# Kernel optimization log

Measured on AMD Instinct MI355X. Metric: run time of the kernel, lower is better.

## Reference

```python
import jax, jax.numpy as jnp
import numpy as np

HEADS = 2
BN_EPS = 1e-5


def _upsample2x_bilinear_ac(x):
    # torch nn.Upsample(scale_factor=2, mode='bilinear', align_corners=True)
    B, C, H, W = x.shape

    def grid(n):
        c = jnp.arange(2 * n) * ((n - 1) / (2 * n - 1))  # align_corners mapping
        i0 = jnp.clip(jnp.floor(c).astype(jnp.int32), 0, n - 2)
        w = (c - i0).astype(x.dtype)
        return i0, w

    i0, wh = grid(H)
    j0, ww = grid(W)
    x = x[:, :, i0, :] * (1 - wh)[None, None, :, None] + x[:, :, i0 + 1, :] * wh[None, None, :, None]
    x = x[:, :, :, j0] * (1 - ww) + x[:, :, :, j0 + 1] * ww
    return x


def _self_attn(x, wq, wkv, wo, wob):
    # x: (b, t, d); lucidrains axial_attention SelfAttention
    b, t, d = x.shape
    e = d // HEADS
    q = x @ wq
    k, v = jnp.split(x @ wkv, 2, axis=-1)
    mh = lambda z: z.reshape(b, t, HEADS, e).transpose(0, 2, 1, 3)  # (b,h,t,e)
    q, k, v = mh(q), mh(k), mh(v)
    dots = jnp.einsum('bhie,bhje->bhij', q, k) * (e ** -0.5)
    attn = jax.nn.softmax(dots, axis=-1)
    o = jnp.einsum('bhij,bhje->bhie', attn, v)
    o = o.transpose(0, 2, 1, 3).reshape(b, t, d)
    return o @ wo + wob


def setup_inputs() -> dict:
    key = jax.random.key(0)
    ks = jax.random.split(key, 16)
    C, E = 256, 128
    cat = 2 * C + E
    s = 0.02
    inp = {
        'x': jax.random.normal(ks[0], (4, C, 64, 64), jnp.float32),
        'res': jax.random.normal(ks[1], (4, E, 128, 128), jnp.float32),
        'wq_h': jax.random.normal(ks[2], (C, C), jnp.float32) * s,
        'wkv_h': jax.random.normal(ks[3], (C, 2 * C), jnp.float32) * s,
        'wo_h': jax.random.normal(ks[4], (C, C), jnp.float32) * s,
        'wob_h': jnp.zeros((C,), jnp.float32),
        'wq_w': jax.random.normal(ks[5], (C, C), jnp.float32) * s,
        'wkv_w': jax.random.normal(ks[6], (C, 2 * C), jnp.float32) * s,
        'wo_w': jax.random.normal(ks[7], (C, C), jnp.float32) * s,
        'wob_w': jnp.zeros((C,), jnp.float32),
        'conv_w': jax.random.normal(ks[8], (cat, E), jnp.float32) * s,
        'gamma': jnp.ones((E,), jnp.float32),
        'beta': jnp.zeros((E,), jnp.float32),
    }
    return inp


def reference(x, res, wq_h, wkv_h, wo_h, wob_h, wq_w, wkv_w, wo_w, wob_w, conv_w, gamma, beta):
    xu = _upsample2x_bilinear_ac(x)  # (B,C,2H,2W)
    B, C, H, W = xu.shape
    # axial attention along H (rows): batch over B*W
    ah = xu.transpose(0, 3, 2, 1).reshape(B * W, H, C)
    ah = _self_attn(ah, wq_h, wkv_h, wo_h, wob_h).reshape(B, W, H, C).transpose(0, 3, 2, 1)
    # axial attention along W (cols): batch over B*H
    aw = xu.transpose(0, 2, 3, 1).reshape(B * H, W, C)
    aw = _self_attn(aw, wq_w, wkv_w, wo_w, wob_w).reshape(B, H, W, C).transpose(0, 3, 1, 2)
    x_attn = jax.nn.relu(ah + aw)  # sum_axial_out=True, then ReLU
    cat = jnp.concatenate([x_attn, xu, res], axis=1)  # (B, 2C+E, H, W)
    y = jnp.einsum('bchw,ce->behw', cat, conv_w)  # conv1x1, no bias
    y = jax.nn.relu(y)
    # BatchNorm2d, training-mode batch stats (biased variance)
    mu = y.mean(axis=(0, 2, 3), keepdims=True)
    var = y.var(axis=(0, 2, 3), keepdims=True)
    y = (y - mu) / jnp.sqrt(var + BN_EPS)
    return y * gamma[None, :, None, None] + beta[None, :, None, None]
```

## Files before the change

kernel.cpp:

```cpp
#include <hip/hip_runtime.h>
#include <hip/hip_bf16.h>
#include <cstdio>


typedef short bf16x8 __attribute__((ext_vector_type(8)));
typedef short bf16x4 __attribute__((ext_vector_type(4)));
typedef float f32x4 __attribute__((ext_vector_type(4)));

#define MFMA16(a, b, c) __builtin_amdgcn_mfma_f32_16x16x32_bf16((a), (b), (c), 0, 0, 0)

__device__ __forceinline__ short f2bf(float v) {
  __hip_bfloat16 h = __float2bfloat16(v);
  union { __hip_bfloat16 h; short s; } u; u.h = h; return u.s;
}
__device__ __forceinline__ float bf2f(short s) {
  return __uint_as_float(((unsigned int)(unsigned short)s) << 16);
}
__device__ __forceinline__ int swz(int row, int col) {
  return col ^ ((row & 7) << 3);
}

struct WtAll {
  const float* src[7];
  short* dst[7];
  int K[7], N[7], tile0[7];
};

__global__ __launch_bounds__(256) void k_wt_all(WtAll P) {
  const int bid = blockIdx.x;
  int i = 0;
#pragma unroll
  for (int j = 1; j < 7; j++) if (bid >= P.tile0[j]) i = j;
  const float* src = P.src[i];
  short* dst = P.dst[i];
  const int K = P.K[i], N = P.N[i];
  const int local = bid - P.tile0[i];
  const int ktiles = K >> 5;
  const int nt = local / ktiles, kt = local - nt * ktiles;
  const int k0 = kt * 32, n0 = nt * 32;
  __shared__ float tile[32][33];
  const int tx = threadIdx.x & 31, ty = threadIdx.x >> 5;
#pragma unroll
  for (int r = 0; r < 4; r++)
    tile[ty + r * 8][tx] = src[(size_t)(k0 + ty + r * 8) * N + n0 + tx];
  __syncthreads();
#pragma unroll
  for (int r = 0; r < 4; r++)
    dst[(size_t)(n0 + ty + r * 8) * K + k0 + tx] = f2bf(tile[tx][ty + r * 8]);
}

__global__ __launch_bounds__(256) void k_upsample(const float* __restrict__ x,
                                                  short* __restrict__ xu) {
  __shared__ float ldsV[64][65];
  const int bh = blockIdx.x, z = blockIdx.y;
  const int b = bh >> 7, h = bh & 127;
  const float chf = h * (63.0f / 127.0f);
  int i0 = (int)chf; if (i0 > 62) i0 = 62;
  const float wh = chf - (float)i0;
  const int t = threadIdx.x;
  const int cbase = z * 64;
  const float* xb = x + ((size_t)(b * 256 + cbase) * 64 + i0) * 64;
#pragma unroll
  for (int p = 0; p < 16; p++) {
    const int li = p * 256 + t;
    const int c = li >> 6, w = li & 63;
    const float* px = xb + (size_t)c * 4096 + w;
    const float v0 = px[0], v1 = px[64];
    ldsV[c][w] = v0 * (1.f - wh) + v1 * wh;
  }
  __syncthreads();
  const int cg = t & 7, wi = t >> 3;
  short* xout = xu + (size_t)(bh * 128) * 256 + cbase + cg * 8;
#pragma unroll
  for (int p = 0; p < 4; p++) {
    const int w = p * 32 + wi;
    const float cwf = w * (63.0f / 127.0f);
    int j0 = (int)cwf; if (j0 > 62) j0 = 62;
    const float ww = cwf - (float)j0;
    bf16x8 o;
#pragma unroll
    for (int u = 0; u < 8; u++) {
      const float v0 = ldsV[cg * 8 + u][j0], v1 = ldsV[cg * 8 + u][j0 + 1];
      o[u] = f2bf(v0 * (1.f - ww) + v1 * ww);
    }
    *(bf16x8*)(xout + (size_t)w * 256) = o;
  }
}

__global__ __launch_bounds__(512, 2) void k_fused(const short* __restrict__ xu,
                                                  const short* __restrict__ wqkvT,
                                                  const short* __restrict__ woT,
                                                  const float* __restrict__ wob,
                                                  short* __restrict__ accb,
                                                  int dir) {
  __shared__ __align__(16) short Xs[128][256];
  __shared__ __align__(16) short Qb[128][128];
  __shared__ __align__(16) short Kb[128][128];
  __shared__ __align__(16) short Vtb[128][128];

  const int s = blockIdx.x;
  const int b = s >> 7, pos = s & 127;
  const int tok0 = b * 16384 + (dir ? pos * 128 : pos);
  const int tstep = dir ? 1 : 128;
  const int tid = threadIdx.x;
  const int lane = tid & 63, wid = tid >> 6;
  const int lr = lane & 15, kb = lane >> 4;
  const int ct = wid * 16;
  const float scale = 0.08838834764831845f;

#pragma unroll
  for (int p = 0; p < 8; p++) {
    const int u = p * 512 + tid;
    const int row = u >> 5, ck = (u & 31) * 8;
    bf16x8 v = *(const bf16x8*)(xu + (size_t)(tok0 + row * tstep) * 256 + ck);
    *(bf16x8*)&Xs[row][swz(row, ck)] = v;
  }

  f32x4 accp[2][8];
#pragma unroll
  for (int i = 0; i < 2; i++)
#pragma unroll
    for (int j = 0; j < 8; j++) accp[i][j] = (f32x4){0.f, 0.f, 0.f, 0.f};

  for (int h = 0; h < 2; h++) {
    const short* wqb = wqkvT + (size_t)(h * 128 + ct + lr) * 256 + kb * 8;
    const short* wkb = wqkvT + (size_t)(256 + h * 128 + ct + lr) * 256 + kb * 8;
    const short* wvb = wqkvT + (size_t)(512 + h * 128 + ct + lr) * 256 + kb * 8;
    bf16x8 wq[8], wk[8], wv[8];
#pragma unroll
    for (int ks = 0; ks < 8; ks++) {
      wq[ks] = *(const bf16x8*)(wqb + ks * 32);
      wk[ks] = *(const bf16x8*)(wkb + ks * 32);
      wv[ks] = *(const bf16x8*)(wvb + ks * 32);
    }

    __syncthreads();

#pragma unroll
    for (int nt = 0; nt < 8; nt++) {
      const int xrow = nt * 16 + lr;
      f32x4 dq = (f32x4){0.f, 0.f, 0.f, 0.f};
      f32x4 dk = (f32x4){0.f, 0.f, 0.f, 0.f};
      f32x4 dv = (f32x4){0.f, 0.f, 0.f, 0.f};
#pragma unroll
      for (int ks = 0; ks < 8; ks++) {
        bf16x8 xf = *(const bf16x8*)&Xs[xrow][swz(xrow, kb * 8 + ks * 32)];
        dq = MFMA16(wq[ks], xf, dq);
        dk = MFMA16(wk[ks], xf, dk);
        dv = MFMA16(xf, wv[ks], dv);
      }
      const int trow = nt * 16 + lr, cc = ct + kb * 4;
      bf16x4 pq = {f2bf(dq[0]), f2bf(dq[1]), f2bf(dq[2]), f2bf(dq[3])};
      bf16x4 pk = {f2bf(dk[0]), f2bf(dk[1]), f2bf(dk[2]), f2bf(dk[3])};
      *(bf16x4*)&Qb[trow][swz(trow, cc)] = pq;
      *(bf16x4*)&Kb[trow][swz(trow, cc)] = pk;
      const int vrow = ct + lr;
      bf16x4 pv = {f2bf(dv[0]), f2bf(dv[1]), f2bf(dv[2]), f2bf(dv[3])};
      *(bf16x4*)&Vtb[vrow][swz(vrow, nt * 16 + kb * 4)] = pv;
    }

    __syncthreads();

    f32x4 s8[8];
#pragma unroll
    for (int i = 0; i < 8; i++) s8[i] = (f32x4){0.f, 0.f, 0.f, 0.f};
    const int qrow = ct + lr;
#pragma unroll
    for (int ks = 0; ks < 4; ks++) {
      bf16x8 aq = *(const bf16x8*)&Qb[qrow][swz(qrow, kb * 8 + ks * 32)];
#pragma unroll
      for (int nj = 0; nj < 8; nj++) {
        const int krow = nj * 16 + lr;
        bf16x8 bk = *(const bf16x8*)&Kb[krow][swz(krow, kb * 8 + ks * 32)];
        s8[nj] = MFMA16(bk, aq, s8[nj]);
      }
    }
    {
      float m = s8[0][0];
#pragma unroll
      for (int nj = 0; nj < 8; nj++)
#pragma unroll
        for (int r = 0; r < 4; r++) m = fmaxf(m, s8[nj][r]);
      m = fmaxf(m, __shfl_xor(m, 16));
      m = fmaxf(m, __shfl_xor(m, 32));
      float sum = 0.f;
#pragma unroll
      for (int nj = 0; nj < 8; nj++)
#pragma unroll
        for (int r = 0; r < 4; r++) {
          s8[nj][r] = __expf((s8[nj][r] - m) * scale);
          sum += s8[nj][r];
        }
      sum += __shfl_xor(sum, 16);
      sum += __shfl_xor(sum, 32);
      const float inv = 1.f / sum;
#pragma unroll
      for (int nj = 0; nj < 8; nj++) {
        bf16x4 pp = {f2bf(s8[nj][0] * inv), f2bf(s8[nj][1] * inv),
                     f2bf(s8[nj][2] * inv), f2bf(s8[nj][3] * inv)};
        *(bf16x4*)&Qb[qrow][swz(qrow, nj * 16 + kb * 4)] = pp;
      }
    }

    f32x4 o8[8];
#pragma unroll
    for (int i = 0; i < 8; i++) o8[i] = (f32x4){0.f, 0.f, 0.f, 0.f};
#pragma unroll
    for (int ks = 0; ks < 4; ks++) {
      bf16x8 bp = *(const bf16x8*)&Qb[qrow][swz(qrow, kb * 8 + ks * 32)];
#pragma unroll
      for (int mi = 0; mi < 8; mi++) {
        const int vrow = mi * 16 + lr;
        bf16x8 av = *(const bf16x8*)&Vtb[vrow][swz(vrow, kb * 8 + ks * 32)];
        o8[mi] = MFMA16(av, bp, o8[mi]);
      }
    }

    __syncthreads();

#pragma unroll
    for (int mi = 0; mi < 8; mi++) {
      const int cc = mi * 16 + kb * 4;
      bf16x4 po = {f2bf(o8[mi][0]), f2bf(o8[mi][1]), f2bf(o8[mi][2]), f2bf(o8[mi][3])};
      *(bf16x4*)&Kb[qrow][swz(qrow, cc)] = po;
    }

    __syncthreads();

    {
      const short* w0 = woT + (size_t)(wid * 32 + lr) * 256 + h * 128 + kb * 8;
      const short* w1 = woT + (size_t)(wid * 32 + 16 + lr) * 256 + h * 128 + kb * 8;
      bf16x8 wa[4], wb2[4];
#pragma unroll
      for (int ks = 0; ks < 4; ks++) {
        wa[ks]  = *(const bf16x8*)(w0 + ks * 32);
        wb2[ks] = *(const bf16x8*)(w1 + ks * 32);
      }
#pragma unroll
      for (int nt = 0; nt < 8; nt++) {
        const int trow = nt * 16 + lr;
#pragma unroll
        for (int ks = 0; ks < 4; ks++) {
          bf16x8 bo = *(const bf16x8*)&Kb[trow][swz(trow, kb * 8 + ks * 32)];
          accp[0][nt] = MFMA16(wa[ks], bo, accp[0][nt]);
          accp[1][nt] = MFMA16(wb2[ks], bo, accp[1][nt]);
        }
      }
    }
  }

#pragma unroll
  for (int mi2 = 0; mi2 < 2; mi2++) {
    const int outc = wid * 32 + mi2 * 16 + kb * 4;
    const float b0 = wob[outc], b1 = wob[outc + 1];
    const float b2 = wob[outc + 2], b3 = wob[outc + 3];
#pragma unroll
    for (int nt = 0; nt < 8; nt++) {
      const int token = tok0 + (nt * 16 + lr) * tstep;
      short* op = accb + (size_t)token * 256 + outc;
      float v0 = accp[mi2][nt][0] + b0, v1 = accp[mi2][nt][1] + b1;
      float v2 = accp[mi2][nt][2] + b2, v3 = accp[mi2][nt][3] + b3;
      if (dir) {
        bf16x4 old = *(const bf16x4*)op;
        v0 += bf2f(old[0]); v1 += bf2f(old[1]);
        v2 += bf2f(old[2]); v3 += bf2f(old[3]);
      }
      bf16x4 pv = {f2bf(v0), f2bf(v1), f2bf(v2), f2bf(v3)};
      *(bf16x4*)op = pv;
    }
  }
}

__global__ __launch_bounds__(256) void k_gemm_conv(const short* __restrict__ accb,
                                                   const short* __restrict__ xu,
                                                   const float* __restrict__ res,
                                                   const short* __restrict__ Bt,
                                                   float* __restrict__ ytmp) {
  const int tid = threadIdx.x;
  const int lane = tid & 63, wid = tid >> 6;
  const int lr = lane & 15, kb = lane >> 4;
  const int wr = wid >> 1, wc = wid & 1;
  const int m0 = blockIdx.y * 128;
  f32x4 acc[4][4];
#pragma unroll
  for (int i = 0; i < 4; i++)
#pragma unroll
    for (int j = 0; j < 4; j++) acc[i][j] = (f32x4){0.f, 0.f, 0.f, 0.f};
  const short* arow1 = accb + (size_t)(m0 + wr * 64 + lr) * 256 + kb * 8;
  const short* arow2 = xu + (size_t)(m0 + wr * 64 + lr) * 256 + kb * 8;
  const short* brow = Bt + (size_t)(wc * 64 + lr) * 640 + kb * 8;
#pragma unroll
  for (int ks = 0; ks < 8; ks++) {
    bf16x8 a[4], b[4];
#pragma unroll
    for (int mi = 0; mi < 4; mi++) {
      bf16x8 tv = *(const bf16x8*)(arow1 + (size_t)mi * 16 * 256 + ks * 32);
#pragma unroll
      for (int u = 0; u < 8; u++)
        tv[u] = ((unsigned short)tv[u] & 0x8000u) ? (short)0 : tv[u];
      a[mi] = tv;
    }
#pragma unroll
    for (int nj = 0; nj < 4; nj++)
      b[nj] = *(const bf16x8*)(brow + (size_t)nj * 16 * 640 + ks * 32);
#pragma unroll
    for (int mi = 0; mi < 4; mi++)
#pragma unroll
      for (int nj = 0; nj < 4; nj++)
        acc[mi][nj] = MFMA16(a[mi], b[nj], acc[mi][nj]);
  }
#pragma unroll
  for (int ks = 8; ks < 16; ks++) {
    bf16x8 a[4], b[4];
#pragma unroll
    for (int mi = 0; mi < 4; mi++)
      a[mi] = *(const bf16x8*)(arow2 + (size_t)mi * 16 * 256 + (ks - 8) * 32);
#pragma unroll
    for (int nj = 0; nj < 4; nj++)
      b[nj] = *(const bf16x8*)(brow + (size_t)nj * 16 * 640 + ks * 32);
#pragma unroll
    for (int mi = 0; mi < 4; mi++)
#pragma unroll
      for (int nj = 0; nj < 4; nj++)
        acc[mi][nj] = MFMA16(a[mi], b[nj], acc[mi][nj]);
  }
  const int bC = (m0 >> 14) * 128;
  const int hh = (m0 >> 7) & 127;
#pragma unroll
  for (int ks = 16; ks < 20; ks++) {
    const int e0 = (ks - 16) * 32 + kb * 8;
    bf16x8 a[4], b[4];
#pragma unroll
    for (int mi = 0; mi < 4; mi++) {
      const int wl = wr * 64 + mi * 16 + lr;
      const float* rp = res + ((size_t)(bC + e0) * 128 + hh) * 128 + wl;
      bf16x8 tv;
#pragma unroll
      for (int u = 0; u < 8; u++) tv[u] = f2bf(rp[(size_t)u * 16384]);
      a[mi] = tv;
    }
#pragma unroll
    for (int nj = 0; nj < 4; nj++)
      b[nj] = *(const bf16x8*)(brow + (size_t)nj * 16 * 640 + ks * 32);
#pragma unroll
    for (int mi = 0; mi < 4; mi++)
#pragma unroll
      for (int nj = 0; nj < 4; nj++)
        acc[mi][nj] = MFMA16(a[mi], b[nj], acc[mi][nj]);
  }
#pragma unroll
  for (int mi = 0; mi < 4; mi++) {
    const int rbase = m0 + wr * 64 + mi * 16 + kb * 4;
#pragma unroll
    for (int nj = 0; nj < 4; nj++) {
      const int c = wc * 64 + nj * 16 + lr;
#pragma unroll
      for (int r = 0; r < 4; r++)
        ytmp[(size_t)(rbase + r) * 128 + c] = fmaxf(acc[mi][nj][r], 0.f);
    }
  }
}

__global__ __launch_bounds__(256) void k_bnstats1(const float* __restrict__ y,
                                                  float* __restrict__ partial) {
  const int blk = blockIdx.x, tid = threadIdx.x;
  const int ch = tid & 127, sub = tid >> 7;
  float s = 0.f, s2 = 0.f;
  const float* p = y + (size_t)(blk * 512 + sub) * 128 + ch;
  for (int i = 0; i < 256; i++) {
    float v = p[(size_t)i * 256];
    s += v; s2 += v * v;
  }
  __shared__ float rs[2][128], rs2[2][128];
  rs[sub][ch] = s; rs2[sub][ch] = s2;
  __syncthreads();
  if (tid < 128) {
    partial[(size_t)(blk * 128 + tid) * 2]     = rs[0][tid] + rs[1][tid];
    partial[(size_t)(blk * 128 + tid) * 2 + 1] = rs2[0][tid] + rs2[1][tid];
  }
}

__global__ __launch_bounds__(128) void k_bnstats2(const float* __restrict__ partial,
                                                  float* __restrict__ stats) {
  const int ch = threadIdx.x;
  float s = 0.f, s2 = 0.f;
  for (int i = 0; i < 128; i++) {
    s  += partial[(size_t)(i * 128 + ch) * 2];
    s2 += partial[(size_t)(i * 128 + ch) * 2 + 1];
  }
  const float mu = s * (1.f / 65536.f);
  const float var = s2 * (1.f / 65536.f) - mu * mu;
  stats[ch * 2] = mu;
  stats[ch * 2 + 1] = rsqrtf(var + 1e-5f);
}

__global__ __launch_bounds__(256) void k_bnout(const float* __restrict__ y,
                                               const float* __restrict__ stats,
                                               const float* __restrict__ gamma,
                                               const float* __restrict__ beta,
                                               float* __restrict__ out) {
  const int bh = blockIdx.x;
  const int b = bh >> 7, h = bh & 127;
  const int w = threadIdx.x & 127, eh = threadIdx.x >> 7;
  const float* yp = y + (size_t)(bh * 128 + w) * 128;
  for (int e2 = 0; e2 < 64; e2++) {
    const int e = e2 * 2 + eh;
    const float mu = stats[e * 2], rstd = stats[e * 2 + 1];
    const float v = yp[e];
    out[((size_t)(b * 128 + e) << 14) + h * 128 + w] =
        (v - mu) * rstd * gamma[e] + beta[e];
  }
}

extern "C" void kernel_launch(void* const* d_in, const int* in_sizes, int n_in,
                              void* d_out, int out_size, void* d_ws, size_t ws_size,
                              hipStream_t stream) {
  const float* x      = (const float*)d_in[0];
  const float* res    = (const float*)d_in[1];
  const float* wq_h   = (const float*)d_in[2];
  const float* wkv_h  = (const float*)d_in[3];
  const float* wo_h   = (const float*)d_in[4];
  const float* wob_h  = (const float*)d_in[5];
  const float* wq_w   = (const float*)d_in[6];
  const float* wkv_w  = (const float*)d_in[7];
  const float* wo_w   = (const float*)d_in[8];
  const float* wob_w  = (const float*)d_in[9];
  const float* conv_w = (const float*)d_in[10];
  const float* gamma  = (const float*)d_in[11];
  const float* beta   = (const float*)d_in[12];

  char* ws = (char*)d_ws;
  short* wqkvT[2] = {(short*)(ws + 0), (short*)(ws + 393216)};
  short* woT[2]   = {(short*)(ws + 786432), (short*)(ws + 917504)};
  short* convT    = (short*)(ws + 1048576);
  short* xu       = (short*)(ws + 1245184);
  float* ytmp     = (float*)(ws + 34799616);
  float* partial  = (float*)(ws + 68354048);
  float* stats    = (float*)(ws + 68485120);
  short* accb     = (short*)d_out;
  float* out      = (float*)d_out;

  if (ws_size < 68486144ull)
    fprintf(stderr, "kernel_launch: ws_size %zu too small\n", ws_size);

  WtAll P;
  P.src[0] = wq_h;  P.dst[0] = wqkvT[0];          P.K[0] = 256; P.N[0] = 256; P.tile0[0] = 0;
  P.src[1] = wkv_h; P.dst[1] = wqkvT[0] + 65536;  P.K[1] = 256; P.N[1] = 512; P.tile0[1] = 64;
  P.src[2] = wq_w;  P.dst[2] = wqkvT[1];          P.K[2] = 256; P.N[2] = 256; P.tile0[2] = 192;
  P.src[3] = wkv_w; P.dst[3] = wqkvT[1] + 65536;  P.K[3] = 256; P.N[3] = 512; P.tile0[3] = 256;
  P.src[4] = wo_h;  P.dst[4] = woT[0];            P.K[4] = 256; P.N[4] = 256; P.tile0[4] = 384;
  P.src[5] = wo_w;  P.dst[5] = woT[1];            P.K[5] = 256; P.N[5] = 256; P.tile0[5] = 448;
  P.src[6] = conv_w;P.dst[6] = convT;             P.K[6] = 640; P.N[6] = 128; P.tile0[6] = 512;
  k_wt_all<<<592, 256, 0, stream>>>(P);

  k_upsample<<<dim3(512, 4), 256, 0, stream>>>(x, xu);

  k_fused<<<512, 512, 0, stream>>>(xu, wqkvT[0], woT[0], wob_h, accb, 0);
  k_fused<<<512, 512, 0, stream>>>(xu, wqkvT[1], woT[1], wob_w, accb, 1);

  k_gemm_conv<<<dim3(1, 512), 256, 0, stream>>>(accb, xu, res, convT, ytmp);
  k_bnstats1<<<128, 256, 0, stream>>>(ytmp, partial);
  k_bnstats2<<<1, 128, 0, stream>>>(partial, stats);
  k_bnout<<<512, 256, 0, stream>>>(ytmp, stats, gamma, beta, out);
}
```

Baseline: 253.6 us.

## Run both axial directions in one launch and shuffle attention output into registers

Merges the H and W axial attention launches into a single grid with blockIdx.y selecting the direction, writing each direction to a separate bf16 buffer. The conv GEMM kernel now sums the two buffers and applies the ReLU, so the read-modify-write accumulation in the second pass goes away. The attention output is repacked with wave-level shuffles into MFMA B fragments instead of round-tripping through LDS, which removes two __syncthreads per head. The output projection is restructured so each wave computes all 256 output channels for its 16 tokens, reading every woT row from global memory per wave. This costs an extra intermediate buffer (more workspace and memory traffic) and more repeated weight loads.

```diff
diff --git a/kernel.cpp b/kernel.cpp
--- a/kernel.cpp
+++ b/kernel.cpp
@@ -6,6 +6,7 @@
 typedef short bf16x8 __attribute__((ext_vector_type(8)));
 typedef short bf16x4 __attribute__((ext_vector_type(4)));
 typedef float f32x4 __attribute__((ext_vector_type(4)));
+typedef unsigned int u32x4 __attribute__((ext_vector_type(4)));
 
 #define MFMA16(a, b, c) __builtin_amdgcn_mfma_f32_16x16x32_bf16((a), (b), (c), 0, 0, 0)
 
@@ -15,6 +16,10 @@
 }
 __device__ __forceinline__ float bf2f(short s) {
   return __uint_as_float(((unsigned int)(unsigned short)s) << 16);
+}
+__device__ __forceinline__ unsigned pk2(float lo, float hi) {
+  return ((unsigned)(unsigned short)f2bf(lo)) |
+         (((unsigned)(unsigned short)f2bf(hi)) << 16);
 }
 __device__ __forceinline__ int swz(int row, int col) {
   return col ^ ((row & 7) << 3);
@@ -88,15 +93,22 @@
 }
 
 __global__ __launch_bounds__(512, 2) void k_fused(const short* __restrict__ xu,
-                                                  const short* __restrict__ wqkvT,
-                                                  const short* __restrict__ woT,
-                                                  const float* __restrict__ wob,
-                                                  short* __restrict__ accb,
-                                                  int dir) {
+                                                  const short* __restrict__ wqkvT0,
+                                                  const short* __restrict__ woT0,
+                                                  const float* __restrict__ wob0,
+                                                  const float* __restrict__ wob1,
+                                                  short* __restrict__ accb0,
+                                                  short* __restrict__ accb1) {
   __shared__ __align__(16) short Xs[128][256];
   __shared__ __align__(16) short Qb[128][128];
   __shared__ __align__(16) short Kb[128][128];
   __shared__ __align__(16) short Vtb[128][128];
+
+  const int dir = blockIdx.y;
+  const short* wqkvT = wqkvT0 + (size_t)dir * 196608;
+  const short* woT   = woT0 + (size_t)dir * 65536;
+  const float* wob   = dir ? wob1 : wob0;
+  short* accb        = dir ? accb1 : accb0;
 
   const int s = blockIdx.x;
   const int b = s >> 7, pos = s & 127;
@@ -116,11 +128,12 @@
     *(bf16x8*)&Xs[row][swz(row, ck)] = v;
   }
 
-  f32x4 accp[2][8];
-#pragma unroll
-  for (int i = 0; i < 2; i++)
-#pragma unroll
-    for (int j = 0; j < 8; j++) accp[i][j] = (f32x4){0.f, 0.f, 0.f, 0.f};
+  f32x4 accp[16];
+#pragma unroll
+  for (int i = 0; i < 16; i++) accp[i] = (f32x4){0.f, 0.f, 0.f, 0.f};
+
+  const int lsA = lr + (((kb * 2) & 3) << 4);
+  const int lsB = lr + (((kb * 2 + 1) & 3) << 4);
 
   for (int h = 0; h < 2; h++) {
     const short* wqb = wqkvT + (size_t)(h * 128 + ct + lr) * 256 + kb * 8;
@@ -216,62 +229,51 @@
       }
     }
 
-    __syncthreads();
-
+    unsigned po[8][2];
 #pragma unroll
     for (int mi = 0; mi < 8; mi++) {
-      const int cc = mi * 16 + kb * 4;
-      bf16x4 po = {f2bf(o8[mi][0]), f2bf(o8[mi][1]), f2bf(o8[mi][2]), f2bf(o8[mi][3])};
-      *(bf16x4*)&Kb[qrow][swz(qrow, cc)] = po;
-    }
-
-    __syncthreads();
-
-    {
-      const short* w0 = woT + (size_t)(wid * 32 + lr) * 256 + h * 128 + kb * 8;
-      const short* w1 = woT + (size_t)(wid * 32 + 16 + lr) * 256 + h * 128 + kb * 8;
-      bf16x8 wa[4], wb2[4];
+      po[mi][0] = pk2(o8[mi][0], o8[mi][1]);
+      po[mi][1] = pk2(o8[mi][2], o8[mi][3]);
+    }
+    bf16x8 bfr[4];
+#pragma unroll
+    for (int mi = 0; mi < 8; mi++) {
+      unsigned loA = (unsigned)__shfl((int)po[mi][0], lsA, 64);
+      unsigned hiA = (unsigned)__shfl((int)po[mi][1], lsA, 64);
+      unsigned loB = (unsigned)__shfl((int)po[mi][0], lsB, 64);
+      unsigned hiB = (unsigned)__shfl((int)po[mi][1], lsB, 64);
+      if ((mi & 1) == (kb >> 1)) {
+        union { u32x4 u; bf16x8 b; } cv;
+        cv.u = (u32x4){loA, hiA, loB, hiB};
+        bfr[mi >> 1] = cv.b;
+      }
+    }
+
+#pragma unroll
+    for (int t = 0; t < 16; t++) {
+      const short* wp = woT + (size_t)(t * 16 + lr) * 256 + h * 128 + kb * 8;
 #pragma unroll
       for (int ks = 0; ks < 4; ks++) {
-        wa[ks]  = *(const bf16x8*)(w0 + ks * 32);
-        wb2[ks] = *(const bf16x8*)(w1 + ks * 32);
-      }
-#pragma unroll
-      for (int nt = 0; nt < 8; nt++) {
-        const int trow = nt * 16 + lr;
-#pragma unroll
-        for (int ks = 0; ks < 4; ks++) {
-          bf16x8 bo = *(const bf16x8*)&Kb[trow][swz(trow, kb * 8 + ks * 32)];
-          accp[0][nt] = MFMA16(wa[ks], bo, accp[0][nt]);
-          accp[1][nt] = MFMA16(wb2[ks], bo, accp[1][nt]);
-        }
-      }
-    }
-  }
-
-#pragma unroll
-  for (int mi2 = 0; mi2 < 2; mi2++) {
-    const int outc = wid * 32 + mi2 * 16 + kb * 4;
-    const float b0 = wob[outc], b1 = wob[outc + 1];
-    const float b2 = wob[outc + 2], b3 = wob[outc + 3];
-#pragma unroll
-    for (int nt = 0; nt < 8; nt++) {
-      const int token = tok0 + (nt * 16 + lr) * tstep;
-      short* op = accb + (size_t)token * 256 + outc;
-      float v0 = accp[mi2][nt][0] + b0, v1 = accp[mi2][nt][1] + b1;
-      float v2 = accp[mi2][nt][2] + b2, v3 = accp[mi2][nt][3] + b3;
-      if (dir) {
-        bf16x4 old = *(const bf16x4*)op;
-        v0 += bf2f(old[0]); v1 += bf2f(old[1]);
-        v2 += bf2f(old[2]); v3 += bf2f(old[3]);
-      }
-      bf16x4 pv = {f2bf(v0), f2bf(v1), f2bf(v2), f2bf(v3)};
-      *(bf16x4*)op = pv;
-    }
-  }
-}
-
-__global__ __launch_bounds__(256) void k_gemm_conv(const short* __restrict__ accb,
+        bf16x8 w = *(const bf16x8*)(wp + ks * 32);
+        accp[t] = MFMA16(w, bfr[ks], accp[t]);
+      }
+    }
+  }
+
+  const int token = tok0 + (ct + lr) * tstep;
+#pragma unroll
+  for (int t = 0; t < 16; t++) {
+    const int outc = t * 16 + kb * 4;
+    bf16x4 pv = {f2bf(accp[t][0] + wob[outc]),
+                 f2bf(accp[t][1] + wob[outc + 1]),
+                 f2bf(accp[t][2] + wob[outc + 2]),
+                 f2bf(accp[t][3] + wob[outc + 3])};
+    *(bf16x4*)(accb + (size_t)token * 256 + outc) = pv;
+  }
+}
+
+__global__ __launch_bounds__(256) void k_gemm_conv(const short* __restrict__ accb0,
+                                                   const short* __restrict__ accb1,
                                                    const short* __restrict__ xu,
                                                    const float* __restrict__ res,
                                                    const short* __restrict__ Bt,
@@ -286,7 +288,8 @@
   for (int i = 0; i < 4; i++)
 #pragma unroll
     for (int j = 0; j < 4; j++) acc[i][j] = (f32x4){0.f, 0.f, 0.f, 0.f};
-  const short* arow1 = accb + (size_t)(m0 + wr * 64 + lr) * 256 + kb * 8;
+  const short* arow0 = accb0 + (size_t)(m0 + wr * 64 + lr) * 256 + kb * 8;
+  const short* arow1 = accb1 + (size_t)(m0 + wr * 64 + lr) * 256 + kb * 8;
   const short* arow2 = xu + (size_t)(m0 + wr * 64 + lr) * 256 + kb * 8;
   const short* brow = Bt + (size_t)(wc * 64 + lr) * 640 + kb * 8;
 #pragma unroll
@@ -294,10 +297,14 @@
     bf16x8 a[4], b[4];
 #pragma unroll
     for (int mi = 0; mi < 4; mi++) {
-      bf16x8 tv = *(const bf16x8*)(arow1 + (size_t)mi * 16 * 256 + ks * 32);
-#pragma unroll
-      for (int u = 0; u < 8; u++)
-        tv[u] = ((unsigned short)tv[u] & 0x8000u) ? (short)0 : tv[u];
+      bf16x8 t0 = *(const bf16x8*)(arow0 + (size_t)mi * 16 * 256 + ks * 32);
+      bf16x8 t1 = *(const bf16x8*)(arow1 + (size_t)mi * 16 * 256 + ks * 32);
+      bf16x8 tv;
+#pragma unroll
+      for (int u = 0; u < 8; u++) {
+        float sv = bf2f(t0[u]) + bf2f(t1[u]);
+        tv[u] = f2bf(fmaxf(sv, 0.f));
+      }
       a[mi] = tv;
     }
 #pragma unroll
@@ -437,10 +444,11 @@
   float* ytmp     = (float*)(ws + 34799616);
   float* partial  = (float*)(ws + 68354048);
   float* stats    = (float*)(ws + 68485120);
-  short* accb     = (short*)d_out;
+  short* accb1    = (short*)(ws + 68486144);
+  short* accb0    = (short*)d_out;
   float* out      = (float*)d_out;
 
-  if (ws_size < 68486144ull)
+  if (ws_size < 102040576ull)
     fprintf(stderr, "kernel_launch: ws_size %zu too small\n", ws_size);
 
   WtAll P;
@@ -455,10 +463,10 @@
 
   k_upsample<<<dim3(512, 4), 256, 0, stream>>>(x, xu);
 
-  k_fused<<<512, 512, 0, stream>>>(xu, wqkvT[0], woT[0], wob_h, accb, 0);
-  k_fused<<<512, 512, 0, stream>>>(xu, wqkvT[1], woT[1], wob_w, accb, 1);
-
-  k_gemm_conv<<<dim3(1, 512), 256, 0, stream>>>(accb, xu, res, convT, ytmp);
+  k_fused<<<dim3(512, 2), 512, 0, stream>>>(xu, wqkvT[0], woT[0],
+                                            wob_h, wob_w, accb0, accb1);
+
+  k_gemm_conv<<<dim3(1, 512), 256, 0, stream>>>(accb0, accb1, xu, res, convT, ytmp);
   k_bnstats1<<<128, 256, 0, stream>>>(ytmp, partial);
   k_bnstats2<<<1, 128, 0, stream>>>(partial, stats);
   k_bnout<<<512, 256, 0, stream>>>(ytmp, stats, gamma, beta, out);
```

Measured after the change: 357.0 us. 1.41x slower.

## Run both axial directions in one launch and fuse BN stats into conv GEMM

Applied to the files above, without the earlier changes.

The two axial-attention launches become one grid with blockIdx.y selecting direction. Each direction now writes its own bf16 buffer instead of read-modify-writing a shared one, and the sum plus ReLU moves into the conv GEMM's A-load. The conv GEMM epilogue also computes per-channel partial sums and sums of squares with shuffles, which removes the separate bnstats1 pass over ytmp. bnout is changed to read ytmp with vector loads. The cost is an extra 33MB workspace buffer, a larger partial reduction in bnstats2, and the added ReLU-sum conversion work inside the GEMM.

```diff
diff --git a/kernel.cpp b/kernel.cpp
--- a/kernel.cpp
+++ b/kernel.cpp
@@ -88,15 +88,22 @@
 }
 
 __global__ __launch_bounds__(512, 2) void k_fused(const short* __restrict__ xu,
-                                                  const short* __restrict__ wqkvT,
-                                                  const short* __restrict__ woT,
-                                                  const float* __restrict__ wob,
-                                                  short* __restrict__ accb,
-                                                  int dir) {
+                                                  const short* __restrict__ wqkvT0,
+                                                  const short* __restrict__ woT0,
+                                                  const float* __restrict__ wob0,
+                                                  const float* __restrict__ wob1,
+                                                  short* __restrict__ accb0,
+                                                  short* __restrict__ accb1) {
   __shared__ __align__(16) short Xs[128][256];
   __shared__ __align__(16) short Qb[128][128];
   __shared__ __align__(16) short Kb[128][128];
   __shared__ __align__(16) short Vtb[128][128];
+
+  const int dir = blockIdx.y;
+  const short* wqkvT = wqkvT0 + (size_t)dir * 196608;
+  const short* woT   = woT0 + (size_t)dir * 65536;
+  const float* wob   = dir ? wob1 : wob0;
+  short* accb        = dir ? accb1 : accb0;
 
   const int s = blockIdx.x;
   const int b = s >> 7, pos = s & 127;
@@ -257,25 +264,21 @@
 #pragma unroll
     for (int nt = 0; nt < 8; nt++) {
       const int token = tok0 + (nt * 16 + lr) * tstep;
-      short* op = accb + (size_t)token * 256 + outc;
-      float v0 = accp[mi2][nt][0] + b0, v1 = accp[mi2][nt][1] + b1;
-      float v2 = accp[mi2][nt][2] + b2, v3 = accp[mi2][nt][3] + b3;
-      if (dir) {
-        bf16x4 old = *(const bf16x4*)op;
-        v0 += bf2f(old[0]); v1 += bf2f(old[1]);
-        v2 += bf2f(old[2]); v3 += bf2f(old[3]);
-      }
-      bf16x4 pv = {f2bf(v0), f2bf(v1), f2bf(v2), f2bf(v3)};
-      *(bf16x4*)op = pv;
-    }
-  }
-}
-
-__global__ __launch_bounds__(256) void k_gemm_conv(const short* __restrict__ accb,
+      bf16x4 pv = {f2bf(accp[mi2][nt][0] + b0), f2bf(accp[mi2][nt][1] + b1),
+                   f2bf(accp[mi2][nt][2] + b2), f2bf(accp[mi2][nt][3] + b3)};
+      *(bf16x4*)(accb + (size_t)token * 256 + outc) = pv;
+    }
+  }
+}
+
+__global__ __launch_bounds__(256) void k_gemm_conv(const short* __restrict__ accb0,
+                                                   const short* __restrict__ accb1,
                                                    const short* __restrict__ xu,
                                                    const float* __restrict__ res,
                                                    const short* __restrict__ Bt,
-                                                   float* __restrict__ ytmp) {
+                                                   float* __restrict__ ytmp,
+                                                   float* __restrict__ partial) {
+  __shared__ float redS[2][128], redS2[2][128];
   const int tid = threadIdx.x;
   const int lane = tid & 63, wid = tid >> 6;
   const int lr = lane & 15, kb = lane >> 4;
@@ -286,7 +289,8 @@
   for (int i = 0; i < 4; i++)
 #pragma unroll
     for (int j = 0; j < 4; j++) acc[i][j] = (f32x4){0.f, 0.f, 0.f, 0.f};
-  const short* arow1 = accb + (size_t)(m0 + wr * 64 + lr) * 256 + kb * 8;
+  const short* arow0 = accb0 + (size_t)(m0 + wr * 64 + lr) * 256 + kb * 8;
+  const short* arow1 = accb1 + (size_t)(m0 + wr * 64 + lr) * 256 + kb * 8;
   const short* arow2 = xu + (size_t)(m0 + wr * 64 + lr) * 256 + kb * 8;
   const short* brow = Bt + (size_t)(wc * 64 + lr) * 640 + kb * 8;
 #pragma unroll
@@ -294,10 +298,14 @@
     bf16x8 a[4], b[4];
 #pragma unroll
     for (int mi = 0; mi < 4; mi++) {
-      bf16x8 tv = *(const bf16x8*)(arow1 + (size_t)mi * 16 * 256 + ks * 32);
-#pragma unroll
-      for (int u = 0; u < 8; u++)
-        tv[u] = ((unsigned short)tv[u] & 0x8000u) ? (short)0 : tv[u];
+      bf16x8 t0 = *(const bf16x8*)(arow0 + (size_t)mi * 16 * 256 + ks * 32);
+      bf16x8 t1 = *(const bf16x8*)(arow1 + (size_t)mi * 16 * 256 + ks * 32);
+      bf16x8 tv;
+#pragma unroll
+      for (int u = 0; u < 8; u++) {
+        float sv = bf2f(t0[u]) + bf2f(t1[u]);
+        tv[u] = f2bf(fmaxf(sv, 0.f));
+      }
       a[mi] = tv;
     }
 #pragma unroll
@@ -349,34 +357,27 @@
         acc[mi][nj] = MFMA16(a[mi], b[nj], acc[mi][nj]);
   }
 #pragma unroll
-  for (int mi = 0; mi < 4; mi++) {
-    const int rbase = m0 + wr * 64 + mi * 16 + kb * 4;
-#pragma unroll
-    for (int nj = 0; nj < 4; nj++) {
-      const int c = wc * 64 + nj * 16 + lr;
-#pragma unroll
-      for (int r = 0; r < 4; r++)
-        ytmp[(size_t)(rbase + r) * 128 + c] = fmaxf(acc[mi][nj][r], 0.f);
-    }
-  }
-}
-
-__global__ __launch_bounds__(256) void k_bnstats1(const float* __restrict__ y,
-                                                  float* __restrict__ partial) {
-  const int blk = blockIdx.x, tid = threadIdx.x;
-  const int ch = tid & 127, sub = tid >> 7;
-  float s = 0.f, s2 = 0.f;
-  const float* p = y + (size_t)(blk * 512 + sub) * 128 + ch;
-  for (int i = 0; i < 256; i++) {
-    float v = p[(size_t)i * 256];
-    s += v; s2 += v * v;
-  }
-  __shared__ float rs[2][128], rs2[2][128];
-  rs[sub][ch] = s; rs2[sub][ch] = s2;
+  for (int nj = 0; nj < 4; nj++) {
+    float s = 0.f, s2 = 0.f;
+    const int c = wc * 64 + nj * 16 + lr;
+#pragma unroll
+    for (int mi = 0; mi < 4; mi++) {
+      const int rbase = m0 + wr * 64 + mi * 16 + kb * 4;
+#pragma unroll
+      for (int r = 0; r < 4; r++) {
+        const float yv = fmaxf(acc[mi][nj][r], 0.f);
+        ytmp[(size_t)(rbase + r) * 128 + c] = yv;
+        s += yv; s2 += yv * yv;
+      }
+    }
+    s += __shfl_xor(s, 16);  s += __shfl_xor(s, 32);
+    s2 += __shfl_xor(s2, 16); s2 += __shfl_xor(s2, 32);
+    if (kb == 0) { redS[wr][c] = s; redS2[wr][c] = s2; }
+  }
   __syncthreads();
   if (tid < 128) {
-    partial[(size_t)(blk * 128 + tid) * 2]     = rs[0][tid] + rs[1][tid];
-    partial[(size_t)(blk * 128 + tid) * 2 + 1] = rs2[0][tid] + rs2[1][tid];
+    partial[((size_t)blockIdx.y * 128 + tid) * 2]     = redS[0][tid] + redS[1][tid];
+    partial[((size_t)blockIdx.y * 128 + tid) * 2 + 1] = redS2[0][tid] + redS2[1][tid];
   }
 }
 
@@ -384,7 +385,7 @@
                                                   float* __restrict__ stats) {
   const int ch = threadIdx.x;
   float s = 0.f, s2 = 0.f;
-  for (int i = 0; i < 128; i++) {
+  for (int i = 0; i < 512; i++) {
     s  += partial[(size_t)(i * 128 + ch) * 2];
     s2 += partial[(size_t)(i * 128 + ch) * 2 + 1];
   }
@@ -401,14 +402,18 @@
                                                float* __restrict__ out) {
   const int bh = blockIdx.x;
   const int b = bh >> 7, h = bh & 127;
-  const int w = threadIdx.x & 127, eh = threadIdx.x >> 7;
-  const float* yp = y + (size_t)(bh * 128 + w) * 128;
-  for (int e2 = 0; e2 < 64; e2++) {
-    const int e = e2 * 2 + eh;
-    const float mu = stats[e * 2], rstd = stats[e * 2 + 1];
-    const float v = yp[e];
-    out[((size_t)(b * 128 + e) << 14) + h * 128 + w] =
-        (v - mu) * rstd * gamma[e] + beta[e];
+  const int w = threadIdx.x & 127, half = threadIdx.x >> 7;
+  const float* yp = y + (size_t)(bh * 128 + w) * 128 + half * 64;
+  float* op = out + ((size_t)(b * 128) << 14) + h * 128 + w;
+#pragma unroll
+  for (int e4 = 0; e4 < 16; e4++) {
+    f32x4 v = *(const f32x4*)(yp + e4 * 4);
+#pragma unroll
+    for (int u = 0; u < 4; u++) {
+      const int e = half * 64 + e4 * 4 + u;
+      const float mu = stats[e * 2], rstd = stats[e * 2 + 1];
+      op[(size_t)e << 14] = (v[u] - mu) * rstd * gamma[e] + beta[e];
+    }
   }
 }
 
@@ -436,11 +441,12 @@
   short* xu       = (short*)(ws + 1245184);
   float* ytmp     = (float*)(ws + 34799616);
   float* partial  = (float*)(ws + 68354048);
-  float* stats    = (float*)(ws + 68485120);
-  short* accb     = (short*)d_out;
+  float* stats    = (float*)(ws + 68878336);
+  short* accb1    = (short*)(ws + 68879360);
+  short* accb0    = (short*)d_out;
   float* out      = (float*)d_out;
 
-  if (ws_size < 68486144ull)
+  if (ws_size < 102433792ull)
     fprintf(stderr, "kernel_launch: ws_size %zu too small\n", ws_size);
 
   WtAll P;
@@ -455,11 +461,11 @@
 
   k_upsample<<<dim3(512, 4), 256, 0, stream>>>(x, xu);
 
-  k_fused<<<512, 512, 0, stream>>>(xu, wqkvT[0], woT[0], wob_h, accb, 0);
-  k_fused<<<512, 512, 0, stream>>>(xu, wqkvT[1], woT[1], wob_w, accb, 1);
-
-  k_gemm_conv<<<dim3(1, 512), 256, 0, stream>>>(accb, xu, res, convT, ytmp);
-  k_bnstats1<<<128, 256, 0, stream>>>(ytmp, partial);
+  k_fused<<<dim3(512, 2), 512, 0, stream>>>(xu, wqkvT[0], woT[0],
+                                            wob_h, wob_w, accb0, accb1);
+
+  k_gemm_conv<<<dim3(1, 512), 256, 0, stream>>>(accb0, accb1, xu, res, convT,
+                                                ytmp, partial);
   k_bnstats2<<<1, 128, 0, stream>>>(partial, stats);
   k_bnout<<<512, 256, 0, stream>>>(ytmp, stats, gamma, beta, out);
 }
```

Measured after the change: 247.9 us (median of 2 runs). -2.3%, faster.
